# Kernel optimization log

Hardware: AMD Instinct MI355X
Metric: run time of the kernel (lower is better)

## Reference

```python
import jax, jax.numpy as jnp
import numpy as np

B, S, H, NH = 2, 2048, 1024, 16
HD = H // NH  # 64


def setup_inputs() -> dict:
    key = jax.random.key(0)
    ks = jax.random.split(key, 9)
    s = 1.0 / np.sqrt(H)
    d = {"x": jax.random.normal(ks[0], (B, S, H), jnp.float32)}
    for i, n in enumerate(["Wq", "Wk", "Wv", "Wo"]):
        d[n] = jax.random.normal(ks[1 + i], (H, H), jnp.float32) * s
    for i, n in enumerate(["bq", "bk", "bv", "bo"]):
        d[n] = jax.random.normal(ks[5 + i], (H,), jnp.float32) * s
    return d


def _heads(x, W, b):
    # torch nn.Linear: y = x @ W.T + b, then split heads -> (B, NH, S, HD)
    y = x @ W.T + b
    return y.reshape(B, S, NH, HD).transpose(0, 2, 1, 3)


def _tetra_channels(t):
    # tetrapoint vector [a, 1-a, a*(1-a), clamp(1-(a+(1-a)),0,1)] for a scalar slice t
    a = jax.nn.sigmoid(t)
    na = 1.0 - a
    neither = jnp.clip(1.0 - (a + na), 0.0, 1.0)
    return jnp.stack([a, na, a * na, neither], axis=-1)  # (..., 4)


def reference(x, Wq, bq, Wk, bk, Wv, bv, Wo, bo):
    Q = _heads(x, Wq, bq)  # (B, NH, S, HD)
    K = _heads(x, Wk, bk)
    V = _heads(x, Wv, bv)
    # Original indexes Q_tetrapoints[:, :, :, 0] on [B,NH,S,HD,4]: selects head-dim
    # slot 0 (resp. 2) and keeps the 4 tetrapoint channels -> (B, NH, S, 4).
    Qa = _tetra_channels(Q[..., 0])
    Ka = _tetra_channels(K[..., 0])
    Qb = _tetra_channels(Q[..., 2])
    Kb = _tetra_channels(K[..., 2])
    scores = (jnp.einsum('bhsc,bhtc->bhst', Qa, Ka) / np.sqrt(HD)
              + 0.1 * jnp.einsum('bhsc,bhtc->bhst', Qb, Kb))  # (B, NH, S, S)
    w = jax.nn.softmax(scores, axis=-1)
    out = jnp.einsum('bhst,bhtd->bhsd', w, V)  # (B, NH, S, HD)
    out = out.transpose(0, 2, 1, 3).reshape(B, S, H)
    return out @ Wo.T + bo
```

## Files before the change

### kernel.cpp

```cpp
#include <hip/hip_runtime.h>
#include <hip/hip_bf16.h>

#define SS 2048
#define HH 1024
#define NHH 16
#define HDD 64

using f32x4  = __attribute__((ext_vector_type(4))) float;
using bf16x8 = __attribute__((ext_vector_type(8))) short;

__device__ __forceinline__ unsigned short f2bf(float f) {
    unsigned u = __builtin_bit_cast(unsigned, f);
    unsigned r = u + 0x7FFFu + ((u >> 16) & 1u);
    return (unsigned short)(r >> 16);
}

__device__ __forceinline__ unsigned bfround(float f) {
    unsigned u = __builtin_bit_cast(unsigned, f);
    return u + 0x7FFFu + ((u >> 16) & 1u);
}
__device__ __forceinline__ unsigned pack2bf(float a, float b) {
    return __builtin_amdgcn_perm(bfround(b), bfround(a), 0x07060302u);
}

__device__ __forceinline__ void tetra(float t, float* c) {
    float a = 1.f / (1.f + __expf(-t));
    float na = 1.f - a;
    float nei = 1.f - (a + na);
    nei = fminf(fmaxf(nei, 0.f), 1.f);
    c[0] = a; c[1] = na; c[2] = a * na; c[3] = nei;
}

__global__ __launch_bounds__(256) void cvt_kernel(
    const float* __restrict__ x, const float* __restrict__ Wv, const float* __restrict__ Wo,
    const float* __restrict__ Wq, const float* __restrict__ Wk,
    const float* __restrict__ bq, const float* __restrict__ bk,
    unsigned short* __restrict__ xb, unsigned short* __restrict__ Wvb, unsigned short* __restrict__ Wob,
    unsigned short* __restrict__ wselb, float* __restrict__ bselws)
{
    if (blockIdx.x >= 2048) {
        int n = blockIdx.x - 2048;
        int h = n >> 2, q = n & 3;
        int rowIdx = h * HDD + ((q & 1) ? 2 : 0);
        const float* src  = (q & 2) ? Wk : Wq;
        const float* bsrc = (q & 2) ? bk : bq;
        int t = threadIdx.x;
        float4 v = *(const float4*)(src + (size_t)rowIdx * HH + t * 4);
        uint2 pk;
        pk.x = pack2bf(v.x, v.y);
        pk.y = pack2bf(v.z, v.w);
        *(uint2*)(wselb + (size_t)n * HH + t * 4) = pk;
        if (t == 0) bselws[n] = bsrc[rowIdx];
        return;
    }
    size_t gid = (size_t)blockIdx.x * 256 + threadIdx.x;
    size_t base = gid * 8;
    {
        float4 a = *(const float4*)(x + base);
        float4 b = *(const float4*)(x + base + 4);
        uint4 pk;
        pk.x = pack2bf(a.x, a.y);
        pk.y = pack2bf(a.z, a.w);
        pk.z = pack2bf(b.x, b.y);
        pk.w = pack2bf(b.z, b.w);
        *(uint4*)(xb + base) = pk;
    }
    if (base < 1048576) {
        float4 a = *(const float4*)(Wv + base);
        float4 b = *(const float4*)(Wv + base + 4);
        uint4 pk;
        pk.x = pack2bf(a.x, a.y);
        pk.y = pack2bf(a.z, a.w);
        pk.z = pack2bf(b.x, b.y);
        pk.w = pack2bf(b.z, b.w);
        *(uint4*)(Wvb + base) = pk;
        a = *(const float4*)(Wo + base);
        b = *(const float4*)(Wo + base + 4);
        pk.x = pack2bf(a.x, a.y);
        pk.y = pack2bf(a.z, a.w);
        pk.z = pack2bf(b.x, b.y);
        pk.w = pack2bf(b.z, b.w);
        *(uint4*)(Wob + base) = pk;
    }
}

__global__ __launch_bounds__(256) void qk_gemm_kernel(
    const unsigned short* __restrict__ xb, const unsigned short* __restrict__ wselb,
    const float* __restrict__ bselws,
    unsigned short* __restrict__ qfb, unsigned short* __restrict__ kfb)
{
    __shared__ unsigned short xs[32][72];
    __shared__ unsigned short ws[64][72];
    __shared__ float ys[32][68];
    int tid = threadIdx.x;
    int wave = tid >> 6, lane = tid & 63;
    int l15 = lane & 15, l16 = lane >> 4;
    int m0 = blockIdx.x * 32;
    int n0w = wave * 16;

    int xr = tid >> 3, xseg = (tid & 7) * 8;
    int wr = tid >> 2, wseg = (tid & 3) * 16;
    const unsigned short* xp = xb + (size_t)(m0 + xr) * HH + xseg;
    const unsigned short* wp = wselb + (size_t)wr * HH + wseg;

    f32x4 acc[2] = {};

    uint4 xv  = *(const uint4*)(xp);
    uint4 wv0 = *(const uint4*)(wp);
    uint4 wv1 = *(const uint4*)(wp + 8);

    for (int k0 = 0; k0 < HH; k0 += 64) {
        __syncthreads();
        *(uint4*)&xs[xr][xseg] = xv;
        *(uint4*)&ws[wr][wseg]     = wv0;
        *(uint4*)&ws[wr][wseg + 8] = wv1;
        __syncthreads();

        int kn = (k0 + 64) & (HH - 1);
        uint4 nxv  = *(const uint4*)(xp + kn);
        uint4 nwv0 = *(const uint4*)(wp + kn);
        uint4 nwv1 = *(const uint4*)(wp + kn + 8);

        #pragma unroll
        for (int kk = 0; kk < 64; kk += 32) {
            bf16x8 bfr = *(const bf16x8*)&ws[n0w + l15][kk + l16 * 8];
            #pragma unroll
            for (int mi = 0; mi < 2; mi++) {
                bf16x8 af = *(const bf16x8*)&xs[mi * 16 + l15][kk + l16 * 8];
                acc[mi] = __builtin_amdgcn_mfma_f32_16x16x32_bf16(af, bfr, acc[mi], 0, 0, 0);
            }
        }
        xv = nxv; wv0 = nwv0; wv1 = nwv1;
    }

    float bias = bselws[n0w + l15];
    __syncthreads();
    #pragma unroll
    for (int mi = 0; mi < 2; mi++)
        #pragma unroll
        for (int r = 0; r < 4; r++)
            ys[mi * 16 + l16 * 4 + r][n0w + l15] = acc[mi][r] + bias;
    __syncthreads();

    #pragma unroll
    for (int pass = 0; pass < 2; pass++) {
        int ml = tid & 31;
        int h = (tid >> 5) + pass * 8;
        float4 y4 = *(const float4*)&ys[ml][h * 4];
        float qa[4], qb2[4], ka[4], kb2[4];
        tetra(y4.x, qa);
        tetra(y4.y, qb2);
        tetra(y4.z, ka);
        tetra(y4.w, kb2);
        int m = m0 + ml, b = m >> 11, s = m & 2047;
        size_t base = ((size_t)(b * NHH + h) * SS + s) * 8;
        uint4 qp, kp;
        qp.x = pack2bf(qa[0] * 0.125f, qa[1] * 0.125f);
        qp.y = pack2bf(qa[2] * 0.125f, qa[3] * 0.125f);
        qp.z = pack2bf(qb2[0] * 0.1f, qb2[1] * 0.1f);
        qp.w = pack2bf(qb2[2] * 0.1f, qb2[3] * 0.1f);
        kp.x = pack2bf(ka[0], ka[1]);
        kp.y = pack2bf(ka[2], ka[3]);
        kp.z = pack2bf(kb2[0], kb2[1]);
        kp.w = pack2bf(kb2[2], kb2[3]);
        *(uint4*)(qfb + base) = qp;
        *(uint4*)(kfb + base) = kp;
    }
}

template<int OUT_MODE>
__global__ __launch_bounds__(256) void gemm_mfma(
    const unsigned short* __restrict__ A, const unsigned short* __restrict__ Bw,
    const float* __restrict__ bias, void* __restrict__ Cout)
{
    __shared__ unsigned short As[128][72];
    __shared__ unsigned short Bs[64][72];
    int tid = threadIdx.x;
    int wave = tid >> 6, lane = tid & 63;
    int l15 = lane & 15, l16 = lane >> 4;
    int wm = wave >> 1, wn = wave & 1;
    int m0 = blockIdx.y * 128, n0 = blockIdx.x * 64;

    int ar = tid >> 1, aseg = (tid & 1) * 32;
    int br = tid >> 2, bseg = (tid & 3) * 16;
    const unsigned short* Ap = A + (size_t)(m0 + ar) * HH + aseg;
    const unsigned short* Bp = Bw + (size_t)(n0 + br) * HH + bseg;

    f32x4 acc[4][2] = {};

    uint4 a0 = *(const uint4*)(Ap);
    uint4 a1 = *(const uint4*)(Ap + 8);
    uint4 a2 = *(const uint4*)(Ap + 16);
    uint4 a3 = *(const uint4*)(Ap + 24);
    uint4 b0 = *(const uint4*)(Bp);
    uint4 b1 = *(const uint4*)(Bp + 8);

    for (int k0 = 0; k0 < HH; k0 += 64) {
        __syncthreads();
        *(uint4*)&As[ar][aseg]      = a0;
        *(uint4*)&As[ar][aseg + 8]  = a1;
        *(uint4*)&As[ar][aseg + 16] = a2;
        *(uint4*)&As[ar][aseg + 24] = a3;
        *(uint4*)&Bs[br][bseg]      = b0;
        *(uint4*)&Bs[br][bseg + 8]  = b1;
        __syncthreads();

        int kn = (k0 + 64) & (HH - 1);
        uint4 na0 = *(const uint4*)(Ap + kn);
        uint4 na1 = *(const uint4*)(Ap + kn + 8);
        uint4 na2 = *(const uint4*)(Ap + kn + 16);
        uint4 na3 = *(const uint4*)(Ap + kn + 24);
        uint4 nb0 = *(const uint4*)(Bp + kn);
        uint4 nb1 = *(const uint4*)(Bp + kn + 8);

        #pragma unroll
        for (int kk = 0; kk < 64; kk += 32) {
            bf16x8 af[4], bfr[2];
            #pragma unroll
            for (int mi = 0; mi < 4; mi++)
                af[mi] = *(const bf16x8*)&As[wm * 64 + mi * 16 + l15][kk + l16 * 8];
            #pragma unroll
            for (int ni = 0; ni < 2; ni++)
                bfr[ni] = *(const bf16x8*)&Bs[wn * 32 + ni * 16 + l15][kk + l16 * 8];
            #pragma unroll
            for (int mi = 0; mi < 4; mi++)
                #pragma unroll
                for (int ni = 0; ni < 2; ni++)
                    acc[mi][ni] = __builtin_amdgcn_mfma_f32_16x16x32_bf16(af[mi], bfr[ni], acc[mi][ni], 0, 0, 0);
        }
        a0 = na0; a1 = na1; a2 = na2; a3 = na3; b0 = nb0; b1 = nb1;
    }

    float bv[2];
    #pragma unroll
    for (int ni = 0; ni < 2; ni++)
        bv[ni] = bias[n0 + wn * 32 + ni * 16 + l15];

    #pragma unroll
    for (int mi = 0; mi < 4; mi++) {
        #pragma unroll
        for (int ni = 0; ni < 2; ni++) {
            int n = n0 + wn * 32 + ni * 16 + l15;
            if (OUT_MODE == 0) {
                #pragma unroll
                for (int r = 0; r < 4; r++) {
                    int m = m0 + wm * 64 + mi * 16 + l16 * 4 + r;
                    ((float*)Cout)[(size_t)m * HH + n] = acc[mi][ni][r] + bv[ni];
                }
            } else {
                int m = m0 + wm * 64 + mi * 16 + l16 * 4;
                int b = m >> 11, s = m & 2047;
                int h = n >> 6, d = n & 63;
                uint2 pk;
                pk.x = pack2bf(acc[mi][ni][0] + bv[ni], acc[mi][ni][1] + bv[ni]);
                pk.y = pack2bf(acc[mi][ni][2] + bv[ni], acc[mi][ni][3] + bv[ni]);
                *(uint2*)((unsigned short*)Cout + ((size_t)((b * NHH + h) * HDD + d)) * SS + s) = pk;
            }
        }
    }
}

__global__ __launch_bounds__(256) void attn_mfma(
    const unsigned short* __restrict__ qfb, const unsigned short* __restrict__ kfb,
    const unsigned short* __restrict__ Vt, unsigned short* __restrict__ attnb)
{
    __shared__ unsigned short vt[64][72];
    __shared__ unsigned short ps[4][16][72];

    int tid = threadIdx.x;
    int wave = tid >> 6, lane = tid & 63;
    int l15 = lane & 15, l16 = lane >> 4;
    int bh = blockIdx.y, b = bh >> 4, h = bh & 15;
    int s0 = blockIdx.x * 64 + wave * 16;

    bf16x8 bfq = {0,0,0,0,0,0,0,0};
    if (l16 == 0)
        bfq = *(const bf16x8*)(qfb + ((size_t)bh * SS + s0 + l15) * 8);

    const short oneb = 0x3F80;
    bf16x8 ones = {oneb,oneb,oneb,oneb,oneb,oneb,oneb,oneb};

    const unsigned short* kfA = kfb + ((size_t)bh * SS + l15) * 8;
    int vd = tid >> 2, vseg = (tid & 3) * 16;
    const unsigned short* vsrc = Vt + ((size_t)bh * HDD + vd) * SS + vseg;

    f32x4 acc[4] = {};
    f32x4 accl = {};

    uint4 sv0 = *(const uint4*)(vsrc);
    uint4 sv1 = *(const uint4*)(vsrc + 8);
    bf16x8 kfr[4];
    #pragma unroll
    for (int tb = 0; tb < 4; tb++)
        kfr[tb] = *(const bf16x8*)(kfA + (size_t)(tb * 16) * 8);

    for (int t0 = 0; t0 < SS; t0 += 64) {
        __syncthreads();
        *(uint4*)&vt[vd][vseg]     = sv0;
        *(uint4*)&vt[vd][vseg + 8] = sv1;
        __syncthreads();

        int tn = (t0 + 64) & (SS - 1);
        uint4 nv0 = *(const uint4*)(vsrc + tn);
        uint4 nv1 = *(const uint4*)(vsrc + tn + 8);
        bf16x8 nkf[4];
        #pragma unroll
        for (int tb = 0; tb < 4; tb++)
            nkf[tb] = *(const bf16x8*)(kfA + (size_t)(tn + tb * 16) * 8);

        #pragma unroll
        for (int tb = 0; tb < 4; tb++) {
            f32x4 sc = {};
            sc = __builtin_amdgcn_mfma_f32_16x16x32_bf16(kfr[tb], bfq, sc, 0, 0, 0);
            float p0 = __expf(sc[0]);
            float p1 = __expf(sc[1]);
            float p2 = __expf(sc[2]);
            float p3 = __expf(sc[3]);
            uint2 pw;
            pw.x = pack2bf(p0, p1);
            pw.y = pack2bf(p2, p3);
            *(uint2*)&ps[wave][l15][tb * 16 + l16 * 4] = pw;
        }

        #pragma unroll
        for (int tk = 0; tk < 2; tk++) {
            bf16x8 ap = *(const bf16x8*)&ps[wave][l15][tk * 32 + l16 * 8];
            accl = __builtin_amdgcn_mfma_f32_16x16x32_bf16(ap, ones, accl, 0, 0, 0);
            #pragma unroll
            for (int nd = 0; nd < 4; nd++) {
                bf16x8 bv = *(const bf16x8*)&vt[nd * 16 + l15][tk * 32 + l16 * 8];
                acc[nd] = __builtin_amdgcn_mfma_f32_16x16x32_bf16(ap, bv, acc[nd], 0, 0, 0);
            }
        }

        sv0 = nv0; sv1 = nv1;
        #pragma unroll
        for (int tb = 0; tb < 4; tb++) kfr[tb] = nkf[tb];
    }

    #pragma unroll
    for (int r = 0; r < 4; r++) {
        float linv = 1.f / accl[r];
        int q = s0 + l16 * 4 + r;
        size_t row = (size_t)(b * SS + q) * HH + h * HDD;
        #pragma unroll
        for (int nd = 0; nd < 4; nd++)
            attnb[row + nd * 16 + l15] = f2bf(acc[nd][r] * linv);
    }
}

extern "C" void kernel_launch(void* const* d_in, const int* in_sizes, int n_in,
                              void* d_out, int out_size, void* d_ws, size_t ws_size,
                              hipStream_t stream)
{
    const float* x  = (const float*)d_in[0];
    const float* Wq = (const float*)d_in[1];
    const float* Wk = (const float*)d_in[2];
    const float* Wv = (const float*)d_in[3];
    const float* Wo = (const float*)d_in[4];
    const float* bq = (const float*)d_in[5];
    const float* bk = (const float*)d_in[6];
    const float* bv = (const float*)d_in[7];
    const float* bo = (const float*)d_in[8];

    unsigned short* qfb   = (unsigned short*)d_ws;
    unsigned short* kfb   = qfb + 524288;
    unsigned short* xb    = kfb + 524288;
    unsigned short* attnb = xb;
    unsigned short* Wvb   = xb + 4194304;
    unsigned short* Wob   = Wvb + 1048576;
    unsigned short* Vt    = Wob + 1048576;
    unsigned short* wselb  = Vt + 4194304;
    float*          bselws = (float*)(wselb + 65536);

    cvt_kernel<<<2112, 256, 0, stream>>>(x, Wv, Wo, Wq, Wk, bq, bk, xb, Wvb, Wob, wselb, bselws);
    qk_gemm_kernel<<<128, 256, 0, stream>>>(xb, wselb, bselws, qfb, kfb);
    gemm_mfma<2><<<dim3(16, 32), 256, 0, stream>>>(xb, Wvb, bv, Vt);
    attn_mfma<<<dim3(32, 32), 256, 0, stream>>>(qfb, kfb, Vt, attnb);
    gemm_mfma<0><<<dim3(16, 32), 256, 0, stream>>>(attnb, Wob, bo, (float*)d_out);
}
```

Before: 185.2 us.

## Retile QK and dense GEMMs and fold log2e scale into Q for exp2

The QK-projection kernel drops from 32 to 16 rows per block, doubling its grid so more CUs are occupied. The shared dense GEMM moves from a 128x64 tile with K-step 64 to a 128x128 tile with K-step 32, giving each wave 16 MFMA accumulators for more reuse per LDS load, at the cost of half the blocks and more register pressure. The attention softmax now uses a hardware exp2 intrinsic, with log2(e) folded into the Q scale factors so the score needs no extra multiply before the exponential.

```diff
diff --git a/kernel.cpp b/kernel.cpp
--- a/kernel.cpp
+++ b/kernel.cpp
@@ -8,6 +8,12 @@
 
 using f32x4  = __attribute__((ext_vector_type(4))) float;
 using bf16x8 = __attribute__((ext_vector_type(8))) short;
+
+#if __has_builtin(__builtin_amdgcn_exp2f)
+#define EXP2F __builtin_amdgcn_exp2f
+#else
+#define EXP2F exp2f
+#endif
 
 __device__ __forceinline__ unsigned short f2bf(float f) {
     unsigned u = __builtin_bit_cast(unsigned, f);
@@ -89,46 +95,43 @@
     const float* __restrict__ bselws,
     unsigned short* __restrict__ qfb, unsigned short* __restrict__ kfb)
 {
-    __shared__ unsigned short xs[32][72];
+    __shared__ unsigned short xs[16][72];
     __shared__ unsigned short ws[64][72];
-    __shared__ float ys[32][68];
+    __shared__ float ys[16][68];
     int tid = threadIdx.x;
     int wave = tid >> 6, lane = tid & 63;
     int l15 = lane & 15, l16 = lane >> 4;
-    int m0 = blockIdx.x * 32;
+    int m0 = blockIdx.x * 16;
     int n0w = wave * 16;
 
-    int xr = tid >> 3, xseg = (tid & 7) * 8;
+    int xr = tid >> 4, xseg = (tid & 15) * 4;
     int wr = tid >> 2, wseg = (tid & 3) * 16;
     const unsigned short* xp = xb + (size_t)(m0 + xr) * HH + xseg;
     const unsigned short* wp = wselb + (size_t)wr * HH + wseg;
 
-    f32x4 acc[2] = {};
-
-    uint4 xv  = *(const uint4*)(xp);
+    f32x4 acc = {};
+
+    uint2 xv  = *(const uint2*)(xp);
     uint4 wv0 = *(const uint4*)(wp);
     uint4 wv1 = *(const uint4*)(wp + 8);
 
     for (int k0 = 0; k0 < HH; k0 += 64) {
         __syncthreads();
-        *(uint4*)&xs[xr][xseg] = xv;
+        *(uint2*)&xs[xr][xseg] = xv;
         *(uint4*)&ws[wr][wseg]     = wv0;
         *(uint4*)&ws[wr][wseg + 8] = wv1;
         __syncthreads();
 
         int kn = (k0 + 64) & (HH - 1);
-        uint4 nxv  = *(const uint4*)(xp + kn);
+        uint2 nxv  = *(const uint2*)(xp + kn);
         uint4 nwv0 = *(const uint4*)(wp + kn);
         uint4 nwv1 = *(const uint4*)(wp + kn + 8);
 
         #pragma unroll
         for (int kk = 0; kk < 64; kk += 32) {
             bf16x8 bfr = *(const bf16x8*)&ws[n0w + l15][kk + l16 * 8];
-            #pragma unroll
-            for (int mi = 0; mi < 2; mi++) {
-                bf16x8 af = *(const bf16x8*)&xs[mi * 16 + l15][kk + l16 * 8];
-                acc[mi] = __builtin_amdgcn_mfma_f32_16x16x32_bf16(af, bfr, acc[mi], 0, 0, 0);
-            }
+            bf16x8 af  = *(const bf16x8*)&xs[l15][kk + l16 * 8];
+            acc = __builtin_amdgcn_mfma_f32_16x16x32_bf16(af, bfr, acc, 0, 0, 0);
         }
         xv = nxv; wv0 = nwv0; wv1 = nwv1;
     }
@@ -136,16 +139,13 @@
     float bias = bselws[n0w + l15];
     __syncthreads();
     #pragma unroll
-    for (int mi = 0; mi < 2; mi++)
-        #pragma unroll
-        for (int r = 0; r < 4; r++)
-            ys[mi * 16 + l16 * 4 + r][n0w + l15] = acc[mi][r] + bias;
+    for (int r = 0; r < 4; r++)
+        ys[l16 * 4 + r][n0w + l15] = acc[r] + bias;
     __syncthreads();
 
-    #pragma unroll
-    for (int pass = 0; pass < 2; pass++) {
-        int ml = tid & 31;
-        int h = (tid >> 5) + pass * 8;
+    {
+        int ml = tid & 15;
+        int h = tid >> 4;
         float4 y4 = *(const float4*)&ys[ml][h * 4];
         float qa[4], qb2[4], ka[4], kb2[4];
         tetra(y4.x, qa);
@@ -154,11 +154,13 @@
         tetra(y4.w, kb2);
         int m = m0 + ml, b = m >> 11, s = m & 2047;
         size_t base = ((size_t)(b * NHH + h) * SS + s) * 8;
+        const float sA = 0.18033688011112042f;
+        const float sB = 0.14426950408889634f;
         uint4 qp, kp;
-        qp.x = pack2bf(qa[0] * 0.125f, qa[1] * 0.125f);
-        qp.y = pack2bf(qa[2] * 0.125f, qa[3] * 0.125f);
-        qp.z = pack2bf(qb2[0] * 0.1f, qb2[1] * 0.1f);
-        qp.w = pack2bf(qb2[2] * 0.1f, qb2[3] * 0.1f);
+        qp.x = pack2bf(qa[0] * sA, qa[1] * sA);
+        qp.y = pack2bf(qa[2] * sA, qa[3] * sA);
+        qp.z = pack2bf(qb2[0] * sB, qb2[1] * sB);
+        qp.w = pack2bf(qb2[2] * sB, qb2[3] * sB);
         kp.x = pack2bf(ka[0], ka[1]);
         kp.y = pack2bf(ka[2], ka[3]);
         kp.z = pack2bf(kb2[0], kb2[1]);
@@ -173,74 +175,65 @@
     const unsigned short* __restrict__ A, const unsigned short* __restrict__ Bw,
     const float* __restrict__ bias, void* __restrict__ Cout)
 {
-    __shared__ unsigned short As[128][72];
-    __shared__ unsigned short Bs[64][72];
+    __shared__ unsigned short As[128][40];
+    __shared__ unsigned short Bs[128][40];
     int tid = threadIdx.x;
     int wave = tid >> 6, lane = tid & 63;
     int l15 = lane & 15, l16 = lane >> 4;
     int wm = wave >> 1, wn = wave & 1;
-    int m0 = blockIdx.y * 128, n0 = blockIdx.x * 64;
-
-    int ar = tid >> 1, aseg = (tid & 1) * 32;
-    int br = tid >> 2, bseg = (tid & 3) * 16;
-    const unsigned short* Ap = A + (size_t)(m0 + ar) * HH + aseg;
-    const unsigned short* Bp = Bw + (size_t)(n0 + br) * HH + bseg;
-
-    f32x4 acc[4][2] = {};
+    int m0 = blockIdx.y * 128, n0 = blockIdx.x * 128;
+
+    int lr = tid >> 1, lseg = (tid & 1) * 16;
+    const unsigned short* Ap = A + (size_t)(m0 + lr) * HH + lseg;
+    const unsigned short* Bp = Bw + (size_t)(n0 + lr) * HH + lseg;
+
+    f32x4 acc[4][4] = {};
 
     uint4 a0 = *(const uint4*)(Ap);
     uint4 a1 = *(const uint4*)(Ap + 8);
-    uint4 a2 = *(const uint4*)(Ap + 16);
-    uint4 a3 = *(const uint4*)(Ap + 24);
     uint4 b0 = *(const uint4*)(Bp);
     uint4 b1 = *(const uint4*)(Bp + 8);
 
-    for (int k0 = 0; k0 < HH; k0 += 64) {
-        __syncthreads();
-        *(uint4*)&As[ar][aseg]      = a0;
-        *(uint4*)&As[ar][aseg + 8]  = a1;
-        *(uint4*)&As[ar][aseg + 16] = a2;
-        *(uint4*)&As[ar][aseg + 24] = a3;
-        *(uint4*)&Bs[br][bseg]      = b0;
-        *(uint4*)&Bs[br][bseg + 8]  = b1;
-        __syncthreads();
-
-        int kn = (k0 + 64) & (HH - 1);
+    for (int k0 = 0; k0 < HH; k0 += 32) {
+        __syncthreads();
+        *(uint4*)&As[lr][lseg]     = a0;
+        *(uint4*)&As[lr][lseg + 8] = a1;
+        *(uint4*)&Bs[lr][lseg]     = b0;
+        *(uint4*)&Bs[lr][lseg + 8] = b1;
+        __syncthreads();
+
+        int kn = (k0 + 32) & (HH - 1);
         uint4 na0 = *(const uint4*)(Ap + kn);
         uint4 na1 = *(const uint4*)(Ap + kn + 8);
-        uint4 na2 = *(const uint4*)(Ap + kn + 16);
-        uint4 na3 = *(const uint4*)(Ap + kn + 24);
         uint4 nb0 = *(const uint4*)(Bp + kn);
         uint4 nb1 = *(const uint4*)(Bp + kn + 8);
 
-        #pragma unroll
-        for (int kk = 0; kk < 64; kk += 32) {
-            bf16x8 af[4], bfr[2];
+        bf16x8 af[4], bfr[4];
+        #pragma unroll
+        for (int mi = 0; mi < 4; mi++)
+            af[mi] = *(const bf16x8*)&As[wm * 64 + mi * 16 + l15][l16 * 8];
+        #pragma unroll
+        for (int ni = 0; ni < 4; ni++)
+            bfr[ni] = *(const bf16x8*)&Bs[wn * 64 + ni * 16 + l15][l16 * 8];
+        #pragma unroll
+        for (int mi = 0; mi < 4; mi++)
             #pragma unroll
-            for (int mi = 0; mi < 4; mi++)
-                af[mi] = *(const bf16x8*)&As[wm * 64 + mi * 16 + l15][kk + l16 * 8];
-            #pragma unroll
-            for (int ni = 0; ni < 2; ni++)
-                bfr[ni] = *(const bf16x8*)&Bs[wn * 32 + ni * 16 + l15][kk + l16 * 8];
-            #pragma unroll
-            for (int mi = 0; mi < 4; mi++)
-                #pragma unroll
-                for (int ni = 0; ni < 2; ni++)
-                    acc[mi][ni] = __builtin_amdgcn_mfma_f32_16x16x32_bf16(af[mi], bfr[ni], acc[mi][ni], 0, 0, 0);
-        }
-        a0 = na0; a1 = na1; a2 = na2; a3 = na3; b0 = nb0; b1 = nb1;
-    }
-
-    float bv[2];
-    #pragma unroll
-    for (int ni = 0; ni < 2; ni++)
-        bv[ni] = bias[n0 + wn * 32 + ni * 16 + l15];
+            for (int ni = 0; ni < 4; ni++)
+                acc[mi][ni] = __builtin_amdgcn_mfma_f32_16x16x32_bf16(af[mi], bfr[ni], acc[mi][ni], 0, 0, 0);
+
+        a0 = na0; a1 = na1; b0 = nb0; b1 = nb1;
+    }
+
+    float bv[4];
+    #pragma unroll
+    for (int ni = 0; ni < 4; ni++)
+        bv[ni] = bias[n0 + wn * 64 + ni * 16 + l15];
 
     #pragma unroll
     for (int mi = 0; mi < 4; mi++) {
         #pragma unroll
-        for (int ni = 0; ni < 2; ni++) {
-            int n = n0 + wn * 32 + ni * 16 + l15;
+        for (int ni = 0; ni < 4; ni++) {
+            int n = n0 + wn * 64 + ni * 16 + l15;
             if (OUT_MODE == 0) {
                 #pragma unroll
                 for (int r = 0; r < 4; r++) {
@@ -312,10 +305,10 @@
         for (int tb = 0; tb < 4; tb++) {
             f32x4 sc = {};
             sc = __builtin_amdgcn_mfma_f32_16x16x32_bf16(kfr[tb], bfq, sc, 0, 0, 0);
-            float p0 = __expf(sc[0]);
-            float p1 = __expf(sc[1]);
-            float p2 = __expf(sc[2]);
-            float p3 = __expf(sc[3]);
+            float p0 = EXP2F(sc[0]);
+            float p1 = EXP2F(sc[1]);
+            float p2 = EXP2F(sc[2]);
+            float p3 = EXP2F(sc[3]);
             uint2 pw;
             pw.x = pack2bf(p0, p1);
             pw.y = pack2bf(p2, p3);
@@ -374,8 +367,8 @@
     float*          bselws = (float*)(wselb + 65536);
 
     cvt_kernel<<<2112, 256, 0, stream>>>(x, Wv, Wo, Wq, Wk, bq, bk, xb, Wvb, Wob, wselb, bselws);
-    qk_gemm_kernel<<<128, 256, 0, stream>>>(xb, wselb, bselws, qfb, kfb);
-    gemm_mfma<2><<<dim3(16, 32), 256, 0, stream>>>(xb, Wvb, bv, Vt);
+    qk_gemm_kernel<<<256, 256, 0, stream>>>(xb, wselb, bselws, qfb, kfb);
+    gemm_mfma<2><<<dim3(8, 32), 256, 0, stream>>>(xb, Wvb, bv, Vt);
     attn_mfma<<<dim3(32, 32), 256, 0, stream>>>(qfb, kfb, Vt, attnb);
-    gemm_mfma<0><<<dim3(16, 32), 256, 0, stream>>>(attnb, Wob, bo, (float*)d_out);
-}
+    gemm_mfma<0><<<dim3(8, 32), 256, 0, stream>>>(attnb, Wob, bo, (float*)d_out);
+}
```

Measured after the change: 198.9 us. +7.4%, slower.
